# Kernel tuning notes

Hardware: AMD Instinct MI355X
Metric: run time of the kernel (lower is better)

## Reference

```python
import jax, jax.numpy as jnp
import numpy as np

B, N, D, P_IN, P_OUT = 8, 2048, 32, 8, 4


def setup_inputs() -> dict:
    key = jax.random.key(0)
    k1, k2, k3, k4 = jax.random.split(key, 4)
    U = jax.random.normal(k1, (B, N, D, P_IN), dtype=jnp.float32)
    A = jax.random.uniform(k2, (B, N, N), dtype=jnp.float32)
    W_self = jax.random.normal(k3, (P_IN, P_OUT), dtype=jnp.float32) * 0.01
    W_neigh = jax.random.normal(k4, (P_IN, P_OUT), dtype=jnp.float32) * 0.01
    bias = jnp.zeros((1, 1, 1, P_OUT), dtype=jnp.float32)
    return {"U": U, "A": A, "W_self": W_self, "W_neigh": W_neigh, "bias": bias}


def _stiefel_projection(Y_flat):
    # Polar factor: Y = W S V^T  ->  proj = W V^T (same as Y @ (Y^T Y)^{-1/2})
    u, _, vt = jnp.linalg.svd(Y_flat, full_matrices=False)
    return u @ vt


def reference(U, A, W_self, W_neigh, bias):
    # U: (B,N,d,p_in); A: (B,N,N)
    M_self = jnp.einsum('bndi,io->bndo', U, W_self)
    M_neigh = jnp.einsum('bndi,io->bndo', U, W_neigh)
    # dense neighborhood aggregation: A @ reshape(M_neigh, (B,N,d*p_out))
    M_agg = jnp.einsum('bnm,bmdo->bndo', A, M_neigh)
    Y = jax.nn.relu(M_self + M_agg + bias)
    Y_flat = Y.reshape(B * N, D, P_OUT)
    U_proj = _stiefel_projection(Y_flat)
    return U_proj.reshape(B, N, D, P_OUT)
```

## Files before the change

### kernel.cpp

```cpp
#include <hip/hip_runtime.h>
#include <math.h>

constexpr int B_   = 8;
constexpr int N_   = 2048;
constexpr int D_   = 32;
constexpr int PIN  = 8;
constexpr int POUT = 4;
constexpr int COLS = 128;
constexpr int BM   = 32;
constexpr int BK   = 64;
constexpr int NT   = N_ / BK;

using f32x4  = __attribute__((ext_vector_type(4))) float;
using bf16x8 = __attribute__((ext_vector_type(8))) short;

__device__ __forceinline__ unsigned short f2bf(float f) {
    union { float f; unsigned u; } v; v.f = f;
    unsigned u = v.u + 0x7fffu + ((v.u >> 16) & 1u);
    return (unsigned short)(u >> 16);
}

__global__ __launch_bounds__(256) void mneigh_t_kernel(
    const float* __restrict__ U, const float* __restrict__ Wn,
    const float* __restrict__ Ws, unsigned short* __restrict__ Btg,
    float* __restrict__ Mself)
{
    const int bt = blockIdx.x;
    const int b  = bt >> 6;
    const int n0 = (bt & 63) * 32;
    const int t  = threadIdx.x;
    const int d  = t >> 3;
    const int ns = t & 7;

    float wn[PIN][POUT], ws[PIN][POUT];
#pragma unroll
    for (int p = 0; p < PIN; ++p)
#pragma unroll
        for (int o = 0; o < POUT; ++o) {
            wn[p][o] = Wn[p * POUT + o];
            ws[p][o] = Ws[p * POUT + o];
        }

    union { unsigned short s[4]; int2 v; } ob[POUT];
    const float* Ub = U + (((size_t)(b * N_ + n0 + ns * 4)) * D_ + d) * PIN;
#pragma unroll
    for (int ni = 0; ni < 4; ++ni) {
        const float4 u0 = *(const float4*)(Ub + (size_t)ni * D_ * PIN);
        const float4 u1 = *(const float4*)(Ub + (size_t)ni * D_ * PIN + 4);
        const float uu[8] = {u0.x, u0.y, u0.z, u0.w, u1.x, u1.y, u1.z, u1.w};
        float4 ms;
#pragma unroll
        for (int o = 0; o < POUT; ++o) {
            float sn = 0.f, ss = 0.f;
#pragma unroll
            for (int p = 0; p < PIN; ++p) {
                sn = fmaf(uu[p], wn[p][o], sn);
                ss = fmaf(uu[p], ws[p][o], ss);
            }
            ob[o].s[ni] = f2bf(sn);
            ((float*)&ms)[o] = ss;
        }
        *(float4*)(Mself + ((size_t)(b * N_ + n0 + ns * 4 + ni)) * COLS + d * 4) = ms;
    }
#pragma unroll
    for (int o = 0; o < POUT; ++o) {
        unsigned short* dst =
            Btg + ((size_t)(b * COLS + d * 4 + o)) * N_ + n0 + ns * 4;
        *(int2*)dst = ob[o].v;
    }
}

__global__ __launch_bounds__(512) void gemm_proj_kernel(
    const float* __restrict__ A, const unsigned short* __restrict__ Btg,
    const float* __restrict__ Mself, const float* __restrict__ bias,
    float* __restrict__ out)
{
    __shared__ unsigned char smem[40960];
    float* Yl = (float*)smem;
    float* Gp = (float*)(smem + 16896);
    float* Sm = (float*)(smem + 22016);

    const int bid = (blockIdx.x & 7) * 64 + (blockIdx.x >> 3);
    const int b   = bid >> 6;
    const int r0  = (bid & 63) * BM;
    const int t   = threadIdx.x;
    const int lane = t & 63, wv = t >> 6;
    const int wr = wv >> 2, wc = wv & 3;
    const int q = lane >> 4, rl = lane & 15;
    const unsigned swz = (unsigned)((lane & 7) << 4);
    const int rA = wr * 16 + rl;

    const int arow = t >> 4, af4 = t & 15;
    const unsigned aswz = (unsigned)((arow & 7) << 4);
    const int bcol = t >> 2, bsg = t & 3;
    const unsigned bswz = (unsigned)((bcol & 7) << 4);

    const float* Ab = A + (size_t)b * N_ * N_ + (size_t)r0 * N_;
    const unsigned short* Bb = Btg + (size_t)b * COLS * N_;
    const float* Mb = Mself + ((size_t)(b * N_ + r0)) * COLS;

    const int cell0 = t, cell1 = t + 512;
    const float4 mpre0 = *(const float4*)(Mb + (size_t)(cell0 >> 5) * COLS + (cell0 & 31) * 4);
    const float4 mpre1 = *(const float4*)(Mb + (size_t)(cell1 >> 5) * COLS + (cell1 & 31) * 4);

    f32x4 acc[2] = {f32x4{0, 0, 0, 0}, f32x4{0, 0, 0, 0}};

    float4 A0, A1; int4 B00, B01, B10, B11;
    A0  = *(const float4*)(Ab + (size_t)arow * N_ + af4 * 4);
    B00 = *(const int4*)(Bb + (size_t)bcol * N_ + bsg * 16);
    B01 = *(const int4*)(Bb + (size_t)bcol * N_ + bsg * 16 + 8);
    A1  = *(const float4*)(Ab + (size_t)arow * N_ + BK + af4 * 4);
    B10 = *(const int4*)(Bb + (size_t)bcol * N_ + BK + bsg * 16);
    B11 = *(const int4*)(Bb + (size_t)bcol * N_ + BK + bsg * 16 + 8);
    {
        union { unsigned short s[4]; int2 v; } pk;
        pk.s[0] = f2bf(A0.x); pk.s[1] = f2bf(A0.y);
        pk.s[2] = f2bf(A0.z); pk.s[3] = f2bf(A0.w);
        *(int2*)(smem + arow * 128 + ((unsigned)(af4 * 8) ^ aswz)) = pk.v;
        *(int4*)(smem + 8192 + bcol * 128 + ((unsigned)(bsg * 32) ^ bswz)) = B00;
        *(int4*)(smem + 8192 + bcol * 128 + ((unsigned)(bsg * 32 + 16) ^ bswz)) = B01;
    }
    asm volatile("s_waitcnt lgkmcnt(0)" ::: "memory");
    __builtin_amdgcn_s_barrier();

#define PIPE_STEP(KT, RA_, RB0_, RB1_, WA_, WB0_, WB1_, CUR)                     \
    {                                                                            \
        const int k2 = ((KT) + 2 < NT) ? ((KT) + 2) * BK : 0;                    \
        RA_  = *(const float4*)(Ab + (size_t)arow * N_ + k2 + af4 * 4);          \
        RB0_ = *(const int4*)(Bb + (size_t)bcol * N_ + k2 + bsg * 16);           \
        RB1_ = *(const int4*)(Bb + (size_t)bcol * N_ + k2 + bsg * 16 + 8);       \
        const unsigned abase = (CUR) * 4096u;                                    \
        const unsigned bbase = 8192u + (CUR) * 16384u;                           \
        __builtin_amdgcn_s_setprio(1);                                           \
        _Pragma("unroll")                                                        \
        for (int ks = 0; ks < 2; ++ks) {                                         \
            const bf16x8 af = *(const bf16x8*)(                                  \
                smem + abase + rA * 128 + ((unsigned)(ks * 64 + q * 16) ^ swz)); \
            _Pragma("unroll")                                                    \
            for (int cf = 0; cf < 2; ++cf) {                                     \
                const int rB = wc * 32 + cf * 16 + rl;                           \
                const bf16x8 bfr = *(const bf16x8*)(                             \
                    smem + bbase + rB * 128 +                                    \
                    ((unsigned)(ks * 64 + q * 16) ^ swz));                       \
                acc[cf] = __builtin_amdgcn_mfma_f32_16x16x32_bf16(               \
                    af, bfr, acc[cf], 0, 0, 0);                                  \
            }                                                                    \
        }                                                                        \
        __builtin_amdgcn_s_setprio(0);                                           \
        {                                                                        \
            union { unsigned short s[4]; int2 v; } pk;                           \
            pk.s[0] = f2bf(WA_.x); pk.s[1] = f2bf(WA_.y);                        \
            pk.s[2] = f2bf(WA_.z); pk.s[3] = f2bf(WA_.w);                        \
            const unsigned nab = ((CUR) ^ 1u) * 4096u;                           \
            const unsigned nbb = 8192u + ((CUR) ^ 1u) * 16384u;                  \
            *(int2*)(smem + nab + arow * 128 +                                   \
                     ((unsigned)(af4 * 8) ^ aswz)) = pk.v;                       \
            *(int4*)(smem + nbb + bcol * 128 +                                   \
                     ((unsigned)(bsg * 32) ^ bswz)) = WB0_;                      \
            *(int4*)(smem + nbb + bcol * 128 +                                   \
                     ((unsigned)(bsg * 32 + 16) ^ bswz)) = WB1_;                 \
        }                                                                        \
        asm volatile("s_waitcnt lgkmcnt(0)" ::: "memory");                       \
        __builtin_amdgcn_s_barrier();                                            \
    }

    for (int kt = 0; kt < NT; kt += 2) {
        PIPE_STEP(kt,     A0, B00, B01, A1, B10, B11, 0u)
        PIPE_STEP(kt + 1, A1, B10, B11, A0, B00, B01, 1u)
    }
#undef PIPE_STEP
    __syncthreads();

#pragma unroll
    for (int cf = 0; cf < 2; ++cf)
#pragma unroll
        for (int r = 0; r < 4; ++r) {
            const int row = wr * 16 + q * 4 + r;
            const int col = wc * 32 + cf * 16 + rl;
            Yl[row * 132 + col] = acc[cf][r];
        }
    __syncthreads();

    const float bz[4] = {bias[0], bias[1], bias[2], bias[3]};
#pragma unroll
    for (int i = 0; i < 2; ++i) {
        const int cell = t + i * 512;
        const int row = cell >> 5, d = cell & 31;
        const float4 m = (i == 0) ? mpre0 : mpre1;
        const int idx = row * 132 + d * 4;
        float4 y = *(const float4*)(Yl + idx);
        y.x = fmaxf(y.x + m.x + bz[0], 0.f);
        y.y = fmaxf(y.y + m.y + bz[1], 0.f);
        y.z = fmaxf(y.z + m.z + bz[2], 0.f);
        y.w = fmaxf(y.w + m.w + bz[3], 0.f);
        *(float4*)(Yl + idx) = y;
    }
    __syncthreads();

    if (t < 128) {
        const int row = t >> 2, qd = t & 3;
        float g[10] = {0,0,0,0,0,0,0,0,0,0};
#pragma unroll
        for (int d = qd * 8; d < qd * 8 + 8; ++d) {
            const float4 y = *(const float4*)(Yl + row * 132 + 4 * d);
            g[0] = fmaf(y.x, y.x, g[0]); g[1] = fmaf(y.x, y.y, g[1]);
            g[2] = fmaf(y.x, y.z, g[2]); g[3] = fmaf(y.x, y.w, g[3]);
            g[4] = fmaf(y.y, y.y, g[4]); g[5] = fmaf(y.y, y.z, g[5]);
            g[6] = fmaf(y.y, y.w, g[6]); g[7] = fmaf(y.z, y.z, g[7]);
            g[8] = fmaf(y.z, y.w, g[8]); g[9] = fmaf(y.w, y.w, g[9]);
        }
        float* gp = Gp + (row * 4 + qd) * 10;
#pragma unroll
        for (int k = 0; k < 10; ++k) gp[k] = g[k];
    }
    __syncthreads();

    if (t < 32) {
        float gg[10];
#pragma unroll
        for (int k = 0; k < 10; ++k)
            gg[k] = Gp[(t * 4 + 0) * 10 + k] + Gp[(t * 4 + 1) * 10 + k] +
                    Gp[(t * 4 + 2) * 10 + k] + Gp[(t * 4 + 3) * 10 + k];
        float m[4][4] = {{gg[0], gg[1], gg[2], gg[3]},
                         {gg[1], gg[4], gg[5], gg[6]},
                         {gg[2], gg[5], gg[7], gg[8]},
                         {gg[3], gg[6], gg[8], gg[9]}};
        float v[4][4] = {{1,0,0,0},{0,1,0,0},{0,0,1,0},{0,0,0,1}};
        for (int sweep = 0; sweep < 6; ++sweep) {
#pragma unroll
            for (int p = 0; p < 3; ++p) {
#pragma unroll
                for (int qq = p + 1; qq < 4; ++qq) {
                    const float apq = m[p][qq];
                    if (fabsf(apq) < 1e-28f) continue;
                    const float theta = (m[qq][qq] - m[p][p]) / (2.f * apq);
                    const float tt = copysignf(1.f, theta) /
                        (fabsf(theta) + sqrtf(fmaf(theta, theta, 1.f)));
                    const float c = 1.f / sqrtf(fmaf(tt, tt, 1.f));
                    const float s = tt * c;
#pragma unroll
                    for (int k = 0; k < 4; ++k) {
                        const float mkp = m[k][p], mkq = m[k][qq];
                        m[k][p] = c * mkp - s * mkq;
                        m[k][qq] = s * mkp + c * mkq;
                    }
#pragma unroll
                    for (int k = 0; k < 4; ++k) {
                        const float mpk = m[p][k], mqk = m[qq][k];
                        m[p][k] = c * mpk - s * mqk;
                        m[qq][k] = s * mpk + c * mqk;
                    }
#pragma unroll
                    for (int k = 0; k < 4; ++k) {
                        const float vkp = v[k][p], vkq = v[k][qq];
                        v[k][p] = c * vkp - s * vkq;
                        v[k][qq] = s * vkp + c * vkq;
                    }
                }
            }
        }
        const float lam[4] = {m[0][0], m[1][1], m[2][2], m[3][3]};
        const float lmax = fmaxf(fmaxf(lam[0], lam[1]), fmaxf(lam[2], lam[3]));
        const float lfloor = fmaxf(lmax * 1e-12f, 1e-30f);
        float rlv[4];
#pragma unroll
        for (int k = 0; k < 4; ++k) rlv[k] = 1.f / sqrtf(fmaxf(lam[k], lfloor));
#pragma unroll
        for (int i = 0; i < 4; ++i)
#pragma unroll
            for (int j = 0; j < 4; ++j)
                Sm[t * 16 + i * 4 + j] =
                    v[i][0] * v[j][0] * rlv[0] + v[i][1] * v[j][1] * rlv[1] +
                    v[i][2] * v[j][2] * rlv[2] + v[i][3] * v[j][3] * rlv[3];
    }
    __syncthreads();

#pragma unroll
    for (int i = 0; i < 2; ++i) {
        const int cell = t + i * 512;
        const int row = cell >> 5, d = cell & 31;
        const float4 y = *(const float4*)(Yl + row * 132 + 4 * d);
        const float* S = Sm + row * 16;
        float4 o4;
        o4.x = y.x * S[0]  + y.y * S[4]  + y.z * S[8]  + y.w * S[12];
        o4.y = y.x * S[1]  + y.y * S[5]  + y.z * S[9]  + y.w * S[13];
        o4.z = y.x * S[2]  + y.y * S[6]  + y.z * S[10] + y.w * S[14];
        o4.w = y.x * S[3]  + y.y * S[7]  + y.z * S[11] + y.w * S[15];
        *(float4*)(out + ((size_t)(b * N_ + r0 + row)) * COLS + 4 * d) = o4;
    }
}

extern "C" void kernel_launch(void* const* d_in, const int* in_sizes, int n_in,
                              void* d_out, int out_size, void* d_ws, size_t ws_size,
                              hipStream_t stream)
{
    const float* U      = (const float*)d_in[0];
    const float* A      = (const float*)d_in[1];
    const float* Wself  = (const float*)d_in[2];
    const float* Wneigh = (const float*)d_in[3];
    const float* bias   = (const float*)d_in[4];
    float* out = (float*)d_out;

    unsigned short* Btg = (unsigned short*)d_ws;
    float* Mself = (float*)((char*)d_ws + (size_t)B_ * COLS * N_ * 2);

    mneigh_t_kernel<<<B_ * (N_ / 32), 256, 0, stream>>>(U, Wneigh, Wself, Btg,
                                                        Mself);
    gemm_proj_kernel<<<B_ * (N_ / BM), 512, 0, stream>>>(A, Btg, Mself, bias,
                                                         out);
}
```

Baseline: 49.11 us.

## Stream GEMM tiles into LDS with direct global_load_lds DMA

Replaces the register-staged global loads plus LDS stores with global_load_lds 16-byte DMA transfers straight into swizzled LDS buffers for both A (kept fp32) and B. The fp32-to-bf16 conversion of A now happens at fragment-read time using v_cvt_pk_bf16_f32, and the pipeline is restructured into a single loop using vmcnt waits and two barriers per step. This removes VGPR staging and conversion on the load path, at the cost of doubling the LDS footprint for A, an extra barrier per iteration, and M_self loads moved after the main loop instead of being prefetched.

```diff
diff --git a/kernel.cpp b/kernel.cpp
--- a/kernel.cpp
+++ b/kernel.cpp
@@ -18,6 +18,13 @@
     union { float f; unsigned u; } v; v.f = f;
     unsigned u = v.u + 0x7fffu + ((v.u >> 16) & 1u);
     return (unsigned short)(u >> 16);
+}
+
+__device__ __forceinline__ void dma16(const void* g, void* l) {
+    __builtin_amdgcn_global_load_lds(
+        (const __attribute__((address_space(1))) unsigned int*)g,
+        (__attribute__((address_space(3))) unsigned int*)(uintptr_t)l,
+        16, 0, 0);
 }
 
 __global__ __launch_bounds__(256) void mneigh_t_kernel(
@@ -75,7 +82,7 @@
     const float* __restrict__ Mself, const float* __restrict__ bias,
     float* __restrict__ out)
 {
-    __shared__ unsigned char smem[40960];
+    __shared__ unsigned char smem[49152];
     float* Yl = (float*)smem;
     float* Gp = (float*)(smem + 16896);
     float* Sm = (float*)(smem + 22016);
@@ -87,88 +94,79 @@
     const int lane = t & 63, wv = t >> 6;
     const int wr = wv >> 2, wc = wv & 3;
     const int q = lane >> 4, rl = lane & 15;
-    const unsigned swz = (unsigned)((lane & 7) << 4);
+    const unsigned swzA = (unsigned)((lane & 7) << 5);
+    const unsigned swzB = (unsigned)((lane & 7) << 4);
     const int rA = wr * 16 + rl;
 
-    const int arow = t >> 4, af4 = t & 15;
-    const unsigned aswz = (unsigned)((arow & 7) << 4);
-    const int bcol = t >> 2, bsg = t & 3;
-    const unsigned bswz = (unsigned)((bcol & 7) << 4);
-
-    const float* Ab = A + (size_t)b * N_ * N_ + (size_t)r0 * N_;
-    const unsigned short* Bb = Btg + (size_t)b * COLS * N_;
-    const float* Mb = Mself + ((size_t)(b * N_ + r0)) * COLS;
-
-    const int cell0 = t, cell1 = t + 512;
-    const float4 mpre0 = *(const float4*)(Mb + (size_t)(cell0 >> 5) * COLS + (cell0 & 31) * 4);
-    const float4 mpre1 = *(const float4*)(Mb + (size_t)(cell1 >> 5) * COLS + (cell1 & 31) * 4);
+    const char* Ab = (const char*)(A + (size_t)b * N_ * N_ + (size_t)r0 * N_);
+    const char* Bb = (const char*)(Btg + (size_t)b * COLS * N_);
+
+    const int arow = t >> 4;
+    const unsigned ainner =
+        ((unsigned)((t & 15) * 16)) ^ ((unsigned)((arow & 7) << 5));
+    const char* a_src = Ab + (size_t)arow * (N_ * 4) + ainner;
+    const int bcol = t >> 3;
+    const unsigned binner =
+        ((unsigned)((t & 7) * 16)) ^ ((unsigned)((bcol & 7) << 4));
+    const char* b_src0 = Bb + (size_t)bcol * (N_ * 2) + binner;
+    const char* b_src1 = Bb + (size_t)(bcol + 64) * (N_ * 2) + binner;
+
+    unsigned char* a_dst = smem + wv * 1024;
+    unsigned char* b_dst = smem + 16384 + wv * 1024;
+
+#define STAGE(K0, BUF)                                                   \
+    do {                                                                 \
+        dma16(a_src + (size_t)(K0) * 4, a_dst + (BUF) * 8192);           \
+        dma16(b_src0 + (size_t)(K0) * 2, b_dst + (BUF) * 16384);         \
+        dma16(b_src1 + (size_t)(K0) * 2, b_dst + (BUF) * 16384 + 8192);  \
+    } while (0)
 
     f32x4 acc[2] = {f32x4{0, 0, 0, 0}, f32x4{0, 0, 0, 0}};
 
-    float4 A0, A1; int4 B00, B01, B10, B11;
-    A0  = *(const float4*)(Ab + (size_t)arow * N_ + af4 * 4);
-    B00 = *(const int4*)(Bb + (size_t)bcol * N_ + bsg * 16);
-    B01 = *(const int4*)(Bb + (size_t)bcol * N_ + bsg * 16 + 8);
-    A1  = *(const float4*)(Ab + (size_t)arow * N_ + BK + af4 * 4);
-    B10 = *(const int4*)(Bb + (size_t)bcol * N_ + BK + bsg * 16);
-    B11 = *(const int4*)(Bb + (size_t)bcol * N_ + BK + bsg * 16 + 8);
-    {
-        union { unsigned short s[4]; int2 v; } pk;
-        pk.s[0] = f2bf(A0.x); pk.s[1] = f2bf(A0.y);
-        pk.s[2] = f2bf(A0.z); pk.s[3] = f2bf(A0.w);
-        *(int2*)(smem + arow * 128 + ((unsigned)(af4 * 8) ^ aswz)) = pk.v;
-        *(int4*)(smem + 8192 + bcol * 128 + ((unsigned)(bsg * 32) ^ bswz)) = B00;
-        *(int4*)(smem + 8192 + bcol * 128 + ((unsigned)(bsg * 32 + 16) ^ bswz)) = B01;
-    }
-    asm volatile("s_waitcnt lgkmcnt(0)" ::: "memory");
+    STAGE(0, 0);
+    STAGE(BK, 1);
+    asm volatile("s_waitcnt vmcnt(3)" ::: "memory");
     __builtin_amdgcn_s_barrier();
 
-#define PIPE_STEP(KT, RA_, RB0_, RB1_, WA_, WB0_, WB1_, CUR)                     \
-    {                                                                            \
-        const int k2 = ((KT) + 2 < NT) ? ((KT) + 2) * BK : 0;                    \
-        RA_  = *(const float4*)(Ab + (size_t)arow * N_ + k2 + af4 * 4);          \
-        RB0_ = *(const int4*)(Bb + (size_t)bcol * N_ + k2 + bsg * 16);           \
-        RB1_ = *(const int4*)(Bb + (size_t)bcol * N_ + k2 + bsg * 16 + 8);       \
-        const unsigned abase = (CUR) * 4096u;                                    \
-        const unsigned bbase = 8192u + (CUR) * 16384u;                           \
-        __builtin_amdgcn_s_setprio(1);                                           \
-        _Pragma("unroll")                                                        \
-        for (int ks = 0; ks < 2; ++ks) {                                         \
-            const bf16x8 af = *(const bf16x8*)(                                  \
-                smem + abase + rA * 128 + ((unsigned)(ks * 64 + q * 16) ^ swz)); \
-            _Pragma("unroll")                                                    \
-            for (int cf = 0; cf < 2; ++cf) {                                     \
-                const int rB = wc * 32 + cf * 16 + rl;                           \
-                const bf16x8 bfr = *(const bf16x8*)(                             \
-                    smem + bbase + rB * 128 +                                    \
-                    ((unsigned)(ks * 64 + q * 16) ^ swz));                       \
-                acc[cf] = __builtin_amdgcn_mfma_f32_16x16x32_bf16(               \
-                    af, bfr, acc[cf], 0, 0, 0);                                  \
-            }                                                                    \
-        }                                                                        \
-        __builtin_amdgcn_s_setprio(0);                                           \
-        {                                                                        \
-            union { unsigned short s[4]; int2 v; } pk;                           \
-            pk.s[0] = f2bf(WA_.x); pk.s[1] = f2bf(WA_.y);                        \
-            pk.s[2] = f2bf(WA_.z); pk.s[3] = f2bf(WA_.w);                        \
-            const unsigned nab = ((CUR) ^ 1u) * 4096u;                           \
-            const unsigned nbb = 8192u + ((CUR) ^ 1u) * 16384u;                  \
-            *(int2*)(smem + nab + arow * 128 +                                   \
-                     ((unsigned)(af4 * 8) ^ aswz)) = pk.v;                       \
-            *(int4*)(smem + nbb + bcol * 128 +                                   \
-                     ((unsigned)(bsg * 32) ^ bswz)) = WB0_;                      \
-            *(int4*)(smem + nbb + bcol * 128 +                                   \
-                     ((unsigned)(bsg * 32 + 16) ^ bswz)) = WB1_;                 \
-        }                                                                        \
-        asm volatile("s_waitcnt lgkmcnt(0)" ::: "memory");                       \
-        __builtin_amdgcn_s_barrier();                                            \
-    }
-
-    for (int kt = 0; kt < NT; kt += 2) {
-        PIPE_STEP(kt,     A0, B00, B01, A1, B10, B11, 0u)
-        PIPE_STEP(kt + 1, A1, B10, B11, A0, B00, B01, 1u)
-    }
-#undef PIPE_STEP
+    for (int kt = 0; kt < NT; ++kt) {
+        const unsigned cur = (unsigned)(kt & 1);
+        const unsigned abase = cur * 8192u;
+        const unsigned bbase = 16384u + cur * 16384u;
+        __builtin_amdgcn_s_setprio(1);
+#pragma unroll
+        for (int ks = 0; ks < 2; ++ks) {
+            const unsigned aoff = ((unsigned)(ks * 128 + q * 32)) ^ swzA;
+            const float4 alo =
+                *(const float4*)(smem + abase + rA * 256 + aoff);
+            const float4 ahi =
+                *(const float4*)(smem + abase + rA * 256 + aoff + 16);
+            union { unsigned u[4]; bf16x8 v; } af;
+            asm("v_cvt_pk_bf16_f32 %0, %1, %2"
+                : "=v"(af.u[0]) : "v"(alo.x), "v"(alo.y));
+            asm("v_cvt_pk_bf16_f32 %0, %1, %2"
+                : "=v"(af.u[1]) : "v"(alo.z), "v"(alo.w));
+            asm("v_cvt_pk_bf16_f32 %0, %1, %2"
+                : "=v"(af.u[2]) : "v"(ahi.x), "v"(ahi.y));
+            asm("v_cvt_pk_bf16_f32 %0, %1, %2"
+                : "=v"(af.u[3]) : "v"(ahi.z), "v"(ahi.w));
+#pragma unroll
+            for (int cf = 0; cf < 2; ++cf) {
+                const int rB = wc * 32 + cf * 16 + rl;
+                const bf16x8 bfr = *(const bf16x8*)(
+                    smem + bbase + rB * 128 +
+                    (((unsigned)(ks * 64 + q * 16)) ^ swzB));
+                acc[cf] = __builtin_amdgcn_mfma_f32_16x16x32_bf16(
+                    af.v, bfr, acc[cf], 0, 0, 0);
+            }
+        }
+        __builtin_amdgcn_s_setprio(0);
+        __builtin_amdgcn_s_barrier();
+        const int k2 = (kt + 2 < NT) ? (kt + 2) * BK : 0;
+        STAGE(k2, cur);
+        asm volatile("s_waitcnt vmcnt(3)" ::: "memory");
+        __builtin_amdgcn_s_barrier();
+    }
+#undef STAGE
     __syncthreads();
 
 #pragma unroll
@@ -182,11 +180,12 @@
     __syncthreads();
 
     const float bz[4] = {bias[0], bias[1], bias[2], bias[3]};
+    const float* Mb = Mself + ((size_t)(b * N_ + r0)) * COLS;
 #pragma unroll
     for (int i = 0; i < 2; ++i) {
         const int cell = t + i * 512;
         const int row = cell >> 5, d = cell & 31;
-        const float4 m = (i == 0) ? mpre0 : mpre1;
+        const float4 m = *(const float4*)(Mb + (size_t)row * COLS + d * 4);
         const int idx = row * 132 + d * 4;
         float4 y = *(const float4*)(Yl + idx);
         y.x = fmaxf(y.x + m.x + bz[0], 0.f);
```

Result: no change. 50.08 us (+2.0%).
